# Kernel optimization log

Hardware: AMD Instinct MI355X
Metric: run time of the kernel (lower is better)

## Reference

```python
import jax, jax.numpy as jnp
import numpy as np

B, F, D, H = 16384, 39, 16, 2   # batch, fields, embed_dim, heads
VOCAB = 10000                    # per-field vocab
DH = D * H                       # attention output dim per layer (no head split)


def setup_inputs() -> dict:
    key = jax.random.key(0)
    ks = jax.random.split(key, 32)
    def n(k, shape, s=0.05):
        return jax.random.normal(k, shape, jnp.float32) * s
    inp = {"x": jax.random.randint(ks[0], (B, F), 0, VOCAB, dtype=jnp.int32)}
    inp["emb"] = n(ks[1], (F * VOCAB, D))
    idx = 2
    for i, din in enumerate([D, DH, DH]):  # layer0: 16->32, layers 1-2: 32->32
        for nm in ["wq", "wk", "wv", "wr"]:
            inp[f"{nm}{i}"] = n(ks[idx], (din, DH)); idx += 1
    prev = F * DH  # 1248 after flatten
    for i, u in enumerate([128, 64, 32, 1], 1):
        inp[f"w{i}"] = n(ks[idx], (prev, u)); idx += 1
        inp[f"b{i}"] = jnp.zeros((u,), jnp.float32)
        prev = u
    return inp


def reference(x, emb,
              wq0, wk0, wv0, wr0,
              wq1, wk1, wv1, wr1,
              wq2, wk2, wv2, wr2,
              w1, b1, w2, b2, w3, b3, w4, b4):
    offsets = jnp.arange(F, dtype=jnp.int32) * VOCAB
    e = emb[x + offsets]                                   # [B, F, D]
    for wq, wk, wv, wr in [(wq0, wk0, wv0, wr0),
                           (wq1, wk1, wv1, wr1),
                           (wq2, wk2, wv2, wr2)]:
        q = jnp.einsum('bfd,de->bfe', e, wq)               # [B, F, DH]
        k = jnp.einsum('bfd,de->bfe', e, wk)
        v = jnp.einsum('bfd,de->bfe', e, wv)
        att = jax.nn.softmax(jnp.einsum('bfe,bge->bfg', q, k), axis=-1)  # [B,F,F], no scaling
        out = jnp.einsum('bfg,bge->bfe', att, v) + jnp.einsum('bfd,de->bfe', e, wr)
        e = jax.nn.relu(out)
    h = e.reshape(B, F * DH)
    for w, b in [(w1, b1), (w2, b2), (w3, b3)]:
        h = jax.nn.relu(h @ w + b)
    return jax.nn.sigmoid(h @ w4 + b4)                     # [B, 1]
```

## Files before the change

kernel.cpp:

```cpp
#include <hip/hip_runtime.h>
#include <math.h>

#define NF   39
#define NB   16384
#define NVOC 10000

typedef unsigned short u16;
typedef unsigned int   u32;
typedef float f32x4 __attribute__((ext_vector_type(4)));
typedef float f32x2 __attribute__((ext_vector_type(2)));
typedef short s16x8 __attribute__((ext_vector_type(8)));
typedef __bf16 bf16x2 __attribute__((ext_vector_type(2)));

#define E3_U16   20447232u
#define WOFF_W1  9216u
#define NSWZ     179200

__device__ __forceinline__ u32 bfadj(float x){
    u32 u = __float_as_uint(x);
    return u + 0x7fffu + ((u >> 16) & 1u);
}
__device__ __forceinline__ u32 pk2(float a, float b){
    bf16x2 t;
    t[0] = (__bf16)a;
    t[1] = (__bf16)b;
    u32 r; __builtin_memcpy(&r, &t, 4); return r;
}
__device__ __forceinline__ u16 f2bf(float f){ return (u16)(bfadj(f) >> 16); }

__device__ __forceinline__ float fexp2(float x){
#if __has_builtin(__builtin_amdgcn_exp2f)
    return __builtin_amdgcn_exp2f(x);
#else
    return exp2f(x);
#endif
}
__device__ __forceinline__ float frcp(float x){
#if __has_builtin(__builtin_amdgcn_rcpf)
    return __builtin_amdgcn_rcpf(x);
#else
    return 1.f / x;
#endif
}

__device__ __forceinline__ void wave_sync(){
    asm volatile("s_waitcnt lgkmcnt(0)" ::: "memory");
}
__device__ __forceinline__ f32x4 mfma16(s16x8 a, s16x8 b, f32x4 c){
    return __builtin_amdgcn_mfma_f32_16x16x32_bf16(a, b, c, 0, 0, 0);
}
__device__ __forceinline__ void store4(u16* p, f32x4 v){
    *(uint2*)p = make_uint2(pk2(v[0], v[1]), pk2(v[2], v[3]));
}

__device__ __forceinline__ f32x2 pkadd(f32x2 a, f32x2 b){
    f32x2 d; asm("v_pk_add_f32 %0, %1, %2" : "=v"(d) : "v"(a), "v"(b)); return d;
}
__device__ __forceinline__ f32x2 pkmul(f32x2 a, f32x2 b){
    f32x2 d; asm("v_pk_mul_f32 %0, %1, %2" : "=v"(d) : "v"(a), "v"(b)); return d;
}

__device__ __forceinline__ void swap32(u32 &a, u32 &b){
    asm("v_permlane32_swap_b32 %0, %1" : "+v"(a), "+v"(b));
}
__device__ __forceinline__ void swap16(u32 &a, u32 &b){
    asm("v_permlane16_swap_b32 %0, %1" : "+v"(a), "+v"(b));
}
__device__ __forceinline__ s16x8 fragPack(u32 a0, u32 a1, u32 b0, u32 b1){
    swap32(a0, b0); swap16(a0, b0);
    swap32(a1, b1); swap16(a1, b1);
    union { u32 w[4]; s16x8 v; } u;
    u.w[0] = a0; u.w[1] = a1; u.w[2] = b0; u.w[3] = b1;
    return u.v;
}
__device__ __forceinline__ s16x8 fragCC(f32x4 A, f32x4 B){
    return fragPack(pk2(A[0],A[1]), pk2(A[2],A[3]), pk2(B[0],B[1]), pk2(B[2],B[3]));
}
__device__ __forceinline__ s16x8 fragC0(f32x4 A){
    return fragPack(pk2(A[0],A[1]), pk2(A[2],A[3]), 0u, 0u);
}
__device__ __forceinline__ s16x8 fragCCn(f32x4 A, f32x4 B, f32x2 iv){
    f32x2 a01 = pkmul(__builtin_shufflevector(A, A, 0, 1), iv);
    f32x2 a23 = pkmul(__builtin_shufflevector(A, A, 2, 3), iv);
    f32x2 b01 = pkmul(__builtin_shufflevector(B, B, 0, 1), iv);
    f32x2 b23 = pkmul(__builtin_shufflevector(B, B, 2, 3), iv);
    return fragPack(pk2(a01.x,a01.y), pk2(a23.x,a23.y),
                    pk2(b01.x,b01.y), pk2(b23.x,b23.y));
}
__device__ __forceinline__ s16x8 fragC0n(f32x4 A, f32x2 iv){
    f32x2 a01 = pkmul(__builtin_shufflevector(A, A, 0, 1), iv);
    f32x2 a23 = pkmul(__builtin_shufflevector(A, A, 2, 3), iv);
    return fragPack(pk2(a01.x,a01.y), pk2(a23.x,a23.y), 0u, 0u);
}
__device__ __forceinline__ float xadd16(float t){
    u32 a = __float_as_uint(t), b = a;
    swap16(a, b);
    return __uint_as_float(a) + __uint_as_float(b);
}
__device__ __forceinline__ float xadd32(float t){
    u32 a = __float_as_uint(t), b = a;
    swap32(a, b);
    return __uint_as_float(a) + __uint_as_float(b);
}

__global__ void __launch_bounds__(256) swz_kernel(
    const float* __restrict__ wq0, const float* __restrict__ wk0,
    const float* __restrict__ wv0, const float* __restrict__ wr0,
    const float* __restrict__ wq1, const float* __restrict__ wk1,
    const float* __restrict__ wv1, const float* __restrict__ wr1,
    const float* __restrict__ wq2, const float* __restrict__ wk2,
    const float* __restrict__ wv2, const float* __restrict__ wr2,
    const float* __restrict__ w1, const float* __restrict__ w2,
    const float* __restrict__ w3, u16* __restrict__ ws)
{
    int gid = (int)blockIdx.x*256 + (int)threadIdx.x;
    if (gid >= NSWZ) return;
    int w    = gid & 511;
    int lane = w >> 3, j = w & 7;
    int n    = lane & 15, quad = lane >> 4;
    int kin  = quad*8 + j;
    float val;
    if (gid < 9216){
        int l = gid / 3072;
        int rr = gid - l*3072;
        int kind = rr >> 10;
        int a    = (rr >> 9) & 1;
        int din  = l ? 32 : 16;
        const float *WQ, *WK, *WV, *WR;
        if (l == 0){ WQ=wq0; WK=wk0; WV=wv0; WR=wr0; }
        else if (l == 1){ WQ=wq1; WK=wk1; WV=wv1; WR=wr1; }
        else { WQ=wq2; WK=wk2; WV=wv2; WR=wr2; }
        if (kind == 0){
            int dp = a*16 + n;
            float s = 0.f;
            if (dp < din && kin < din){
                float acc = 0.f;
                for (int e = 0; e < 32; ++e)
                    acc += WQ[kin*32 + e] * WK[dp*32 + e];
                s = acc * 1.44269504f;
            }
            val = s;
        } else {
            const float* W = (kind == 1) ? WV : WR;
            val = (kin < din) ? W[kin*32 + a*16 + n] : 0.f;
        }
    } else if (gid < 9216 + 159744){
        int tt = (gid - 9216) >> 9;
        int ks = tt >> 3, nt = tt & 7;
        val = w1[(ks*32 + kin)*128 + nt*16 + n];
    } else if (gid < 9216 + 159744 + 8192){
        int tt = (gid - (9216+159744)) >> 9;
        int ks = tt >> 2, nt = tt & 3;
        val = w2[(ks*32 + kin)*64 + nt*16 + n];
    } else {
        int tt = (gid - (9216+159744+8192)) >> 9;
        int ks = tt >> 1, nt = tt & 1;
        val = w3[(ks*32 + kin)*32 + nt*16 + n];
    }
    ws[E3_U16 + gid] = f2bf(val);
}

__global__ void __launch_bounds__(256, 4) attn_kernel(
    const int* __restrict__ x, const float* __restrict__ emb,
    u16* __restrict__ ws)
{
    __shared__ __align__(16) u16 lds[4*1536];
    const int tid  = (int)threadIdx.x;
    const int wid  = tid >> 6, lane = tid & 63;
    const int h    = lane >> 4, nl = lane & 15;
    const int r    = (int)blockIdx.x*4 + wid;

    u16* eBuf = lds + wid*1536;
    const u16* wmat = ws + E3_U16;
    const f32x4 z = {0.f, 0.f, 0.f, 0.f};

    f32x4 ci;
#pragma unroll
    for (int reg = 0; reg < 4; ++reg)
        ci[reg] = (h*4 + reg >= 7) ? -1e30f : 0.f;

    if (lane < 48){
        int f = lane, mt = f >> 4, fl = f & 15;
        u16* row = eBuf + mt*512 + fl*8;
        if (f < NF){
            const float4* ep = (const float4*)(emb + ((size_t)(x[r*NF + f] + f*NVOC))*16);
            float4 e0 = ep[0], e1 = ep[1], e2 = ep[2], e3 = ep[3];
            *(uint4*)(row)       = make_uint4(pk2(e0.x,e0.y), pk2(e0.z,e0.w),
                                              pk2(e1.x,e1.y), pk2(e1.z,e1.w));
            *(uint4*)(row + 128) = make_uint4(pk2(e2.x,e2.y), pk2(e2.z,e2.w),
                                              pk2(e3.x,e3.y), pk2(e3.z,e3.w));
        } else {
            *(uint4*)(row)       = make_uint4(0,0,0,0);
            *(uint4*)(row + 128) = make_uint4(0,0,0,0);
        }
        *(uint4*)(row + 256) = make_uint4(0,0,0,0);
        *(uint4*)(row + 384) = make_uint4(0,0,0,0);
    }
    wave_sync();
    s16x8 bE[3];
#pragma unroll
    for (int nt = 0; nt < 3; ++nt)
        bE[nt] = *(const s16x8*)(eBuf + nt*512 + lane*8);

#pragma unroll 1
    for (int L = 0; L < 3; ++L){
        const u16* wL = wmat + L*3072;

        s16x8 bT[3];
        {
            s16x8 g0 = *(const s16x8*)(wL +       lane*8);
            s16x8 g1 = *(const s16x8*)(wL + 512 + lane*8);
#pragma unroll
            for (int nt = 0; nt < 3; ++nt)
                bT[nt] = fragCC(mfma16(g0, bE[nt], z), mfma16(g1, bE[nt], z));
        }
        s16x8 aV[2][2];
        {
            s16x8 v0 = *(const s16x8*)(wL + 1024 + lane*8);
            s16x8 v1 = *(const s16x8*)(wL + 1536 + lane*8);
#pragma unroll
            for (int emt = 0; emt < 2; ++emt){
                s16x8 vb = emt ? v1 : v0;
                f32x4 c0 = mfma16(bE[0], vb, z);
                f32x4 c1 = mfma16(bE[1], vb, z);
                f32x4 c2 = mfma16(bE[2], vb, z);
                aV[0][emt] = fragCC(c0, c1);
                aV[1][emt] = fragC0(c2);
            }
        }
        f32x4 S[3][3];
#pragma unroll
        for (int mtg = 0; mtg < 3; ++mtg)
#pragma unroll
        for (int nt = 0; nt < 3; ++nt)
            S[mtg][nt] = mfma16(bE[mtg], bT[nt], (mtg == 2) ? ci : z);

        float inv[3];
#pragma unroll
        for (int nt = 0; nt < 3; ++nt){
            f32x2 acc2 = {0.f, 0.f};
#pragma unroll
            for (int mtg = 0; mtg < 3; ++mtg){
#pragma unroll
                for (int reg = 0; reg < 4; ++reg)
                    S[mtg][nt][reg] = fexp2(S[mtg][nt][reg]);
                acc2 = pkadd(acc2, __builtin_shufflevector(S[mtg][nt], S[mtg][nt], 0, 1));
                acc2 = pkadd(acc2, __builtin_shufflevector(S[mtg][nt], S[mtg][nt], 2, 3));
            }
            inv[nt] = frcp(xadd32(xadd16(acc2.x + acc2.y)));
        }
        inv[2] = (nl < 7) ? inv[2] : 0.f;

        f32x4 R[2][3];
        {
            s16x8 r0 = *(const s16x8*)(wL + 2048 + lane*8);
            s16x8 r1 = *(const s16x8*)(wL + 2560 + lane*8);
#pragma unroll
            for (int nt = 0; nt < 3; ++nt){
                R[0][nt] = mfma16(r0, bE[nt], z);
                R[1][nt] = mfma16(r1, bE[nt], z);
            }
        }
        if (nl >= 7){ R[0][2] = z; R[1][2] = z; }

        if (L < 2){
#pragma unroll
            for (int nt = 0; nt < 3; ++nt){
                f32x2 iv = {inv[nt], inv[nt]};
                s16x8 p0 = fragCCn(S[0][nt], S[1][nt], iv);
                s16x8 p1 = fragC0n(S[2][nt], iv);
                f32x4 oc[2];
#pragma unroll
                for (int emt = 0; emt < 2; ++emt){
                    f32x4 o = mfma16(aV[1][emt], p1,
                              mfma16(aV[0][emt], p0, R[emt][nt]));
#pragma unroll
                    for (int reg = 0; reg < 4; ++reg)
                        o[reg] = fmaxf(o[reg], 0.f);
                    oc[emt] = o;
                }
                bE[nt] = fragCC(oc[0], oc[1]);
            }
        } else {
            int st = r >> 4, sm = r & 15;
            u32 base = (u32)(st*39)*512u + (u32)(sm*8 + (h>>1)*128 + (h&1)*4);
#pragma unroll
            for (int nt = 0; nt < 3; ++nt){
                f32x2 iv = {inv[nt], inv[nt]};
                s16x8 p0 = fragCCn(S[0][nt], S[1][nt], iv);
                s16x8 p1 = fragC0n(S[2][nt], iv);
                int f = nt*16 + nl;
#pragma unroll
                for (int emt = 0; emt < 2; ++emt){
                    f32x4 o = mfma16(aV[1][emt], p1,
                              mfma16(aV[0][emt], p0, R[emt][nt]));
#pragma unroll
                    for (int reg = 0; reg < 4; ++reg)
                        o[reg] = fmaxf(o[reg], 0.f);
                    if (f < NF)
                        *(uint2*)(ws + base + (u32)f*512u + emt*256) =
                            make_uint2(pk2(o[0], o[1]), pk2(o[2], o[3]));
                }
            }
        }
    }
}

__global__ void __launch_bounds__(512, 4) mlp_kernel(
    const float* __restrict__ b1, const float* __restrict__ b2,
    const float* __restrict__ b3, const float* __restrict__ w4,
    const float* __restrict__ b4, const u16* __restrict__ ws,
    float* __restrict__ out)
{
    __shared__ __align__(16) u16 smem[46208];
    u16*   e3s  = smem;
    u16*   h1t  = smem + 39936;
    u16*   h2t  = smem + 44032;
    float* part = (float*)(smem + 46080);

    const int tid = (int)threadIdx.x;
    const int w   = tid >> 6, lane = tid & 63;
    const int h   = lane >> 4, nl = lane & 15;
    const int A_off = nl*8 + (h>>1)*128 + (h&1)*4;

    const u16* w1b = ws + E3_U16 + WOFF_W1;
    const u16* w2b = w1b + 159744u;
    const u16* w3b = w2b + 8192u;
    const f32x4 z = {0.f,0.f,0.f,0.f};

    const u32 e3base = (u32)blockIdx.x * 39936u;
#pragma unroll
    for (int k = 0; k < 10; ++k){
        u32 idx = (u32)tid*8u + (u32)k*4096u;
        if (idx < 39936u)
            *(s16x8*)(e3s + idx) = *(const s16x8*)(ws + e3base + idx);
    }
    __syncthreads();

    {
        f32x4 a0 = z, a1 = z;
#pragma unroll 3
        for (int ks = 0; ks < 39; ++ks){
            s16x8 aW = *(const s16x8*)(w1b + (ks*8 + w)*512 + lane*8);
            s16x8 e0 = *(const s16x8*)(e3s + ks*512 + lane*8);
            s16x8 e1 = *(const s16x8*)(e3s + 19968 + ks*512 + lane*8);
            a0 = mfma16(aW, e0, a0);
            a1 = mfma16(aW, e1, a1);
        }
        float4 bv = *(const float4*)(b1 + w*16 + h*4);
        f32x4 v0, v1;
        v0[0] = fmaxf(a0[0] + bv.x, 0.f); v1[0] = fmaxf(a1[0] + bv.x, 0.f);
        v0[1] = fmaxf(a0[1] + bv.y, 0.f); v1[1] = fmaxf(a1[1] + bv.y, 0.f);
        v0[2] = fmaxf(a0[2] + bv.z, 0.f); v1[2] = fmaxf(a1[2] + bv.z, 0.f);
        v0[3] = fmaxf(a0[3] + bv.w, 0.f); v1[3] = fmaxf(a1[3] + bv.w, 0.f);
        store4(h1t +        w*256 + A_off, v0);
        store4(h1t + 2048 + w*256 + A_off, v1);
    }
    __syncthreads();

    {
        int stg = w >> 2, nt2 = w & 3;
        const u16* h1s = h1t + stg*2048;
        f32x4 a2 = z;
#pragma unroll
        for (int ks = 0; ks < 4; ++ks){
            s16x8 aW = *(const s16x8*)(w2b + (ks*4 + nt2)*512 + lane*8);
            s16x8 bH = *(const s16x8*)(h1s + ks*512 + lane*8);
            a2 = mfma16(aW, bH, a2);
        }
        float4 bv = *(const float4*)(b2 + nt2*16 + h*4);
        f32x4 v;
        v[0] = fmaxf(a2[0] + bv.x, 0.f);
        v[1] = fmaxf(a2[1] + bv.y, 0.f);
        v[2] = fmaxf(a2[2] + bv.z, 0.f);
        v[3] = fmaxf(a2[3] + bv.w, 0.f);
        store4(h2t + stg*1024 + (nt2>>1)*512 + (nt2&1)*256 + A_off, v);
    }
    __syncthreads();

    if ((w & 3) < 2){
        int stg = w >> 2, nt3 = w & 3;
        const u16* h2s = h2t + stg*1024;
        f32x4 a3 = z;
#pragma unroll
        for (int ks = 0; ks < 2; ++ks){
            s16x8 aW = *(const s16x8*)(w3b + (ks*2 + nt3)*512 + lane*8);
            s16x8 bH = *(const s16x8*)(h2s + ks*512 + lane*8);
            a3 = mfma16(aW, bH, a3);
        }
        float4 b3v = *(const float4*)(b3 + nt3*16 + h*4);
        float4 w4v = *(const float4*)(w4 + nt3*16 + h*4);
        float t = fmaxf(a3[0] + b3v.x, 0.f)*w4v.x
                + fmaxf(a3[1] + b3v.y, 0.f)*w4v.y
                + fmaxf(a3[2] + b3v.z, 0.f)*w4v.z
                + fmaxf(a3[3] + b3v.w, 0.f)*w4v.w;
        t += __shfl_xor(t, 16, 64);
        t += __shfl_xor(t, 32, 64);
        if (h == 0) part[stg*32 + nt3*16 + nl] = t;
    }
    __syncthreads();
    if (tid < 32){
        int stg = tid >> 4, sm = tid & 15;
        float zz = part[stg*32 + sm] + part[stg*32 + 16 + sm] + b4[0];
        out[((int)blockIdx.x*2 + stg)*16 + sm] = 1.f/(1.f + __expf(-zz));
    }
}

extern "C" void kernel_launch(void* const* d_in, const int* in_sizes, int n_in,
                              void* d_out, int out_size, void* d_ws, size_t ws_size,
                              hipStream_t stream)
{
    (void)in_sizes; (void)n_in; (void)ws_size; (void)out_size;
    const int*   x   = (const int*)d_in[0];
    const float* emb = (const float*)d_in[1];
    u16* ws = (u16*)d_ws;

    swz_kernel<<<(NSWZ+255)/256, 256, 0, stream>>>(
        (const float*)d_in[2],  (const float*)d_in[3],  (const float*)d_in[4],  (const float*)d_in[5],
        (const float*)d_in[6],  (const float*)d_in[7],  (const float*)d_in[8],  (const float*)d_in[9],
        (const float*)d_in[10], (const float*)d_in[11], (const float*)d_in[12], (const float*)d_in[13],
        (const float*)d_in[14], (const float*)d_in[16], (const float*)d_in[18], ws);

    attn_kernel<<<NB/4, 256, 0, stream>>>(x, emb, ws);

    mlp_kernel<<<NB/32, 512, 0, stream>>>(
        (const float*)d_in[15], (const float*)d_in[17], (const float*)d_in[19],
        (const float*)d_in[20], (const float*)d_in[21], ws, (float*)d_out);
}
```

Before: 177.7 us.

## Process two batch rows per wave in attention kernel for ILP

Each wave now handles two independent samples (r0 and r0+8192) and interleaves their MFMA, exp and reduction chains, while the grid is halved and launch bounds drop to 2 blocks per CU. The aim is to hide MFMA and exp dependency latency through instruction-level parallelism and to amortize the per-layer weight fragment loads over two samples. In exchange it roughly doubles register use and LDS per block, which lowers occupancy.

```diff
diff --git a/kernel.cpp b/kernel.cpp
--- a/kernel.cpp
+++ b/kernel.cpp
@@ -160,17 +160,17 @@
     ws[E3_U16 + gid] = f2bf(val);
 }
 
-__global__ void __launch_bounds__(256, 4) attn_kernel(
+__global__ void __launch_bounds__(256, 2) attn_kernel(
     const int* __restrict__ x, const float* __restrict__ emb,
     u16* __restrict__ ws)
 {
-    __shared__ __align__(16) u16 lds[4*1536];
+    __shared__ __align__(16) u16 lds[4*3072];
     const int tid  = (int)threadIdx.x;
     const int wid  = tid >> 6, lane = tid & 63;
     const int h    = lane >> 4, nl = lane & 15;
-    const int r    = (int)blockIdx.x*4 + wid;
-
-    u16* eBuf = lds + wid*1536;
+    const int r0   = (int)blockIdx.x*4 + wid;
+
+    u16* eBuf = lds + wid*3072;
     const u16* wmat = ws + E3_U16;
     const f32x4 z = {0.f, 0.f, 0.f, 0.f};
 
@@ -179,127 +179,151 @@
     for (int reg = 0; reg < 4; ++reg)
         ci[reg] = (h*4 + reg >= 7) ? -1e30f : 0.f;
 
-    if (lane < 48){
-        int f = lane, mt = f >> 4, fl = f & 15;
-        u16* row = eBuf + mt*512 + fl*8;
-        if (f < NF){
-            const float4* ep = (const float4*)(emb + ((size_t)(x[r*NF + f] + f*NVOC))*16);
-            float4 e0 = ep[0], e1 = ep[1], e2 = ep[2], e3 = ep[3];
-            *(uint4*)(row)       = make_uint4(pk2(e0.x,e0.y), pk2(e0.z,e0.w),
-                                              pk2(e1.x,e1.y), pk2(e1.z,e1.w));
-            *(uint4*)(row + 128) = make_uint4(pk2(e2.x,e2.y), pk2(e2.z,e2.w),
-                                              pk2(e3.x,e3.y), pk2(e3.z,e3.w));
-        } else {
-            *(uint4*)(row)       = make_uint4(0,0,0,0);
-            *(uint4*)(row + 128) = make_uint4(0,0,0,0);
-        }
-        *(uint4*)(row + 256) = make_uint4(0,0,0,0);
-        *(uint4*)(row + 384) = make_uint4(0,0,0,0);
+#pragma unroll
+    for (int s = 0; s < 2; ++s){
+        if (lane < 48){
+            int rr = r0 + s*8192;
+            int f = lane, mt = f >> 4, fl = f & 15;
+            u16* row = eBuf + s*1536 + mt*512 + fl*8;
+            if (f < NF){
+                const float4* ep = (const float4*)(emb + ((size_t)(x[rr*NF + f] + f*NVOC))*16);
+                float4 e0 = ep[0], e1 = ep[1], e2 = ep[2], e3 = ep[3];
+                *(uint4*)(row)       = make_uint4(pk2(e0.x,e0.y), pk2(e0.z,e0.w),
+                                                  pk2(e1.x,e1.y), pk2(e1.z,e1.w));
+                *(uint4*)(row + 128) = make_uint4(pk2(e2.x,e2.y), pk2(e2.z,e2.w),
+                                                  pk2(e3.x,e3.y), pk2(e3.z,e3.w));
+            } else {
+                *(uint4*)(row)       = make_uint4(0,0,0,0);
+                *(uint4*)(row + 128) = make_uint4(0,0,0,0);
+            }
+            *(uint4*)(row + 256) = make_uint4(0,0,0,0);
+            *(uint4*)(row + 384) = make_uint4(0,0,0,0);
+        }
     }
     wave_sync();
-    s16x8 bE[3];
+    s16x8 bE[2][3];
+#pragma unroll
+    for (int s = 0; s < 2; ++s)
 #pragma unroll
     for (int nt = 0; nt < 3; ++nt)
-        bE[nt] = *(const s16x8*)(eBuf + nt*512 + lane*8);
+        bE[s][nt] = *(const s16x8*)(eBuf + s*1536 + nt*512 + lane*8);
 
 #pragma unroll 1
     for (int L = 0; L < 3; ++L){
         const u16* wL = wmat + L*3072;
 
-        s16x8 bT[3];
+        s16x8 bT[2][3];
         {
             s16x8 g0 = *(const s16x8*)(wL +       lane*8);
             s16x8 g1 = *(const s16x8*)(wL + 512 + lane*8);
 #pragma unroll
+            for (int s = 0; s < 2; ++s)
+#pragma unroll
             for (int nt = 0; nt < 3; ++nt)
-                bT[nt] = fragCC(mfma16(g0, bE[nt], z), mfma16(g1, bE[nt], z));
-        }
-        s16x8 aV[2][2];
+                bT[s][nt] = fragCC(mfma16(g0, bE[s][nt], z), mfma16(g1, bE[s][nt], z));
+        }
+        s16x8 aV[2][2][2];
         {
             s16x8 v0 = *(const s16x8*)(wL + 1024 + lane*8);
             s16x8 v1 = *(const s16x8*)(wL + 1536 + lane*8);
 #pragma unroll
+            for (int s = 0; s < 2; ++s)
+#pragma unroll
             for (int emt = 0; emt < 2; ++emt){
                 s16x8 vb = emt ? v1 : v0;
-                f32x4 c0 = mfma16(bE[0], vb, z);
-                f32x4 c1 = mfma16(bE[1], vb, z);
-                f32x4 c2 = mfma16(bE[2], vb, z);
-                aV[0][emt] = fragCC(c0, c1);
-                aV[1][emt] = fragC0(c2);
-            }
-        }
-        f32x4 S[3][3];
+                f32x4 c0 = mfma16(bE[s][0], vb, z);
+                f32x4 c1 = mfma16(bE[s][1], vb, z);
+                f32x4 c2 = mfma16(bE[s][2], vb, z);
+                aV[s][0][emt] = fragCC(c0, c1);
+                aV[s][1][emt] = fragC0(c2);
+            }
+        }
+        f32x4 S[2][3][3];
+#pragma unroll
+        for (int s = 0; s < 2; ++s)
 #pragma unroll
         for (int mtg = 0; mtg < 3; ++mtg)
 #pragma unroll
         for (int nt = 0; nt < 3; ++nt)
-            S[mtg][nt] = mfma16(bE[mtg], bT[nt], (mtg == 2) ? ci : z);
-
-        float inv[3];
-#pragma unroll
-        for (int nt = 0; nt < 3; ++nt){
-            f32x2 acc2 = {0.f, 0.f};
-#pragma unroll
-            for (int mtg = 0; mtg < 3; ++mtg){
-#pragma unroll
-                for (int reg = 0; reg < 4; ++reg)
-                    S[mtg][nt][reg] = fexp2(S[mtg][nt][reg]);
-                acc2 = pkadd(acc2, __builtin_shufflevector(S[mtg][nt], S[mtg][nt], 0, 1));
-                acc2 = pkadd(acc2, __builtin_shufflevector(S[mtg][nt], S[mtg][nt], 2, 3));
-            }
-            inv[nt] = frcp(xadd32(xadd16(acc2.x + acc2.y)));
-        }
-        inv[2] = (nl < 7) ? inv[2] : 0.f;
-
-        f32x4 R[2][3];
+            S[s][mtg][nt] = mfma16(bE[s][mtg], bT[s][nt], (mtg == 2) ? ci : z);
+
+        float inv[2][3];
+#pragma unroll
+        for (int s = 0; s < 2; ++s){
+#pragma unroll
+            for (int nt = 0; nt < 3; ++nt){
+                f32x2 acc2 = {0.f, 0.f};
+#pragma unroll
+                for (int mtg = 0; mtg < 3; ++mtg){
+#pragma unroll
+                    for (int reg = 0; reg < 4; ++reg)
+                        S[s][mtg][nt][reg] = fexp2(S[s][mtg][nt][reg]);
+                    acc2 = pkadd(acc2, __builtin_shufflevector(S[s][mtg][nt], S[s][mtg][nt], 0, 1));
+                    acc2 = pkadd(acc2, __builtin_shufflevector(S[s][mtg][nt], S[s][mtg][nt], 2, 3));
+                }
+                inv[s][nt] = frcp(xadd32(xadd16(acc2.x + acc2.y)));
+            }
+            inv[s][2] = (nl < 7) ? inv[s][2] : 0.f;
+        }
+
+        f32x4 R[2][2][3];
         {
-            s16x8 r0 = *(const s16x8*)(wL + 2048 + lane*8);
-            s16x8 r1 = *(const s16x8*)(wL + 2560 + lane*8);
+            s16x8 w0 = *(const s16x8*)(wL + 2048 + lane*8);
+            s16x8 w1 = *(const s16x8*)(wL + 2560 + lane*8);
+#pragma unroll
+            for (int s = 0; s < 2; ++s){
+#pragma unroll
+                for (int nt = 0; nt < 3; ++nt){
+                    R[s][0][nt] = mfma16(w0, bE[s][nt], z);
+                    R[s][1][nt] = mfma16(w1, bE[s][nt], z);
+                }
+                if (nl >= 7){ R[s][0][2] = z; R[s][1][2] = z; }
+            }
+        }
+
+        if (L < 2){
+#pragma unroll
+            for (int s = 0; s < 2; ++s)
 #pragma unroll
             for (int nt = 0; nt < 3; ++nt){
-                R[0][nt] = mfma16(r0, bE[nt], z);
-                R[1][nt] = mfma16(r1, bE[nt], z);
-            }
-        }
-        if (nl >= 7){ R[0][2] = z; R[1][2] = z; }
-
-        if (L < 2){
-#pragma unroll
-            for (int nt = 0; nt < 3; ++nt){
-                f32x2 iv = {inv[nt], inv[nt]};
-                s16x8 p0 = fragCCn(S[0][nt], S[1][nt], iv);
-                s16x8 p1 = fragC0n(S[2][nt], iv);
+                f32x2 iv = {inv[s][nt], inv[s][nt]};
+                s16x8 p0 = fragCCn(S[s][0][nt], S[s][1][nt], iv);
+                s16x8 p1 = fragC0n(S[s][2][nt], iv);
                 f32x4 oc[2];
 #pragma unroll
                 for (int emt = 0; emt < 2; ++emt){
-                    f32x4 o = mfma16(aV[1][emt], p1,
-                              mfma16(aV[0][emt], p0, R[emt][nt]));
+                    f32x4 o = mfma16(aV[s][1][emt], p1,
+                              mfma16(aV[s][0][emt], p0, R[s][emt][nt]));
 #pragma unroll
                     for (int reg = 0; reg < 4; ++reg)
                         o[reg] = fmaxf(o[reg], 0.f);
                     oc[emt] = o;
                 }
-                bE[nt] = fragCC(oc[0], oc[1]);
+                bE[s][nt] = fragCC(oc[0], oc[1]);
             }
         } else {
-            int st = r >> 4, sm = r & 15;
-            u32 base = (u32)(st*39)*512u + (u32)(sm*8 + (h>>1)*128 + (h&1)*4);
-#pragma unroll
-            for (int nt = 0; nt < 3; ++nt){
-                f32x2 iv = {inv[nt], inv[nt]};
-                s16x8 p0 = fragCCn(S[0][nt], S[1][nt], iv);
-                s16x8 p1 = fragC0n(S[2][nt], iv);
-                int f = nt*16 + nl;
-#pragma unroll
-                for (int emt = 0; emt < 2; ++emt){
-                    f32x4 o = mfma16(aV[1][emt], p1,
-                              mfma16(aV[0][emt], p0, R[emt][nt]));
-#pragma unroll
-                    for (int reg = 0; reg < 4; ++reg)
-                        o[reg] = fmaxf(o[reg], 0.f);
-                    if (f < NF)
-                        *(uint2*)(ws + base + (u32)f*512u + emt*256) =
-                            make_uint2(pk2(o[0], o[1]), pk2(o[2], o[3]));
+#pragma unroll
+            for (int s = 0; s < 2; ++s){
+                int rr = r0 + s*8192;
+                int st = rr >> 4, sm = rr & 15;
+                u32 base = (u32)(st*39)*512u + (u32)(sm*8 + (h>>1)*128 + (h&1)*4);
+#pragma unroll
+                for (int nt = 0; nt < 3; ++nt){
+                    f32x2 iv = {inv[s][nt], inv[s][nt]};
+                    s16x8 p0 = fragCCn(S[s][0][nt], S[s][1][nt], iv);
+                    s16x8 p1 = fragC0n(S[s][2][nt], iv);
+                    int f = nt*16 + nl;
+#pragma unroll
+                    for (int emt = 0; emt < 2; ++emt){
+                        f32x4 o = mfma16(aV[s][1][emt], p1,
+                                  mfma16(aV[s][0][emt], p0, R[s][emt][nt]));
+#pragma unroll
+                        for (int reg = 0; reg < 4; ++reg)
+                            o[reg] = fmaxf(o[reg], 0.f);
+                        if (f < NF)
+                            *(uint2*)(ws + base + (u32)f*512u + emt*256) =
+                                make_uint2(pk2(o[0], o[1]), pk2(o[2], o[3]));
+                    }
                 }
             }
         }
@@ -421,7 +445,7 @@
         (const float*)d_in[10], (const float*)d_in[11], (const float*)d_in[12], (const float*)d_in[13],
         (const float*)d_in[14], (const float*)d_in[16], (const float*)d_in[18], ws);
 
-    attn_kernel<<<NB/4, 256, 0, stream>>>(x, emb, ws);
+    attn_kernel<<<NB/8, 256, 0, stream>>>(x, emb, ws);
 
     mlp_kernel<<<NB/32, 512, 0, stream>>>(
         (const float*)d_in[15], (const float*)d_in[17], (const float*)d_in[19],
```

New measurement: 184.3 us. 1.04x slower.
